# Kernel optimization log

Hardware: AMD Instinct MI355X
Metric: run time of the kernel (lower is better)

Reference implementation:

```python
import jax, jax.numpy as jnp
import numpy as np

V, E, H2, K = 30000, 256, 256, 13  # vocab, embed dim, per-direction hidden, num tags
B, T = 64, 512


def setup_inputs() -> dict:
    key = jax.random.key(0)
    ks = jax.random.split(key, 12)
    s = 0.1
    return {
        "x": jax.random.randint(ks[0], (B, T), 0, V, dtype=jnp.int32),
        "emb": jax.random.normal(ks[1], (V, E), dtype=jnp.float32) * s,
        "w_ih_f": jax.random.normal(ks[2], (4 * H2, E), dtype=jnp.float32) * s,
        "w_hh_f": jax.random.normal(ks[3], (4 * H2, H2), dtype=jnp.float32) * s,
        "b_ih_f": jnp.zeros((4 * H2,), jnp.float32),
        "b_hh_f": jnp.zeros((4 * H2,), jnp.float32),
        "w_ih_b": jax.random.normal(ks[4], (4 * H2, E), dtype=jnp.float32) * s,
        "w_hh_b": jax.random.normal(ks[5], (4 * H2, H2), dtype=jnp.float32) * s,
        "b_ih_b": jnp.zeros((4 * H2,), jnp.float32),
        "b_hh_b": jnp.zeros((4 * H2,), jnp.float32),
        "w_out": jax.random.normal(ks[6], (K, 2 * H2), dtype=jnp.float32) * s,
        "b_out": jnp.zeros((K,), jnp.float32),
        "start_trans": jax.random.normal(ks[7], (K,), dtype=jnp.float32) * s,
        "end_trans": jax.random.normal(ks[8], (K,), dtype=jnp.float32) * s,
        "trans": jax.random.normal(ks[9], (K, K), dtype=jnp.float32) * s,
    }


def _lstm_dir(xg, w_hh, reverse):
    # xg: [T, B, 4H] precomputed input-side gate pre-activations (PyTorch i|f|g|o order)
    Bsz, H = xg.shape[1], w_hh.shape[1]

    def step(carry, g_in):
        h, c = carry
        g = g_in + h @ w_hh.T
        i, f, gg, o = jnp.split(g, 4, axis=-1)
        c = jax.nn.sigmoid(f) * c + jax.nn.sigmoid(i) * jnp.tanh(gg)
        h = jax.nn.sigmoid(o) * jnp.tanh(c)
        return (h, c), h

    init = (jnp.zeros((Bsz, H), xg.dtype), jnp.zeros((Bsz, H), xg.dtype))
    _, hs = jax.lax.scan(step, init, xg, reverse=reverse)
    return hs  # [T, B, H]


def reference(x, emb, w_ih_f, w_hh_f, b_ih_f, b_hh_f, w_ih_b, w_hh_b, b_ih_b, b_hh_b,
              w_out, b_out, start_trans, end_trans, trans):
    e = emb[x].transpose(1, 0, 2)                     # [T, B, E] time-major
    xg_f = e @ w_ih_f.T + (b_ih_f + b_hh_f)           # [T, B, 4H] (fold both biases)
    xg_b = e @ w_ih_b.T + (b_ih_b + b_hh_b)
    h_f = _lstm_dir(xg_f, w_hh_f, reverse=False)
    h_b = _lstm_dir(xg_b, w_hh_b, reverse=True)
    h = jnp.concatenate([h_f, h_b], axis=-1)          # [T, B, 2H]; dropout = identity (eval)
    emissions = h @ w_out.T + b_out                   # [T, B, K]

    # CRF Viterbi decode (torchcrf semantics, full mask)
    score = start_trans + emissions[0]                # [B, K]

    def vstep(score, emit_t):
        s = score[:, :, None] + trans[None] + emit_t[:, None, :]  # [B, K_prev, K_next]
        return s.max(axis=1), s.argmax(axis=1)

    score, bps = jax.lax.scan(vstep, score, emissions[1:])        # bps: [T-1, B, K]
    score = score + end_trans
    best_last = jnp.argmax(score, axis=-1)            # [B]
    best_score = jnp.max(score, axis=-1)              # [B]

    def btstep(tag, bp_t):
        prev = jnp.take_along_axis(bp_t, tag[:, None], axis=1)[:, 0]
        return prev, prev

    _, path_head = jax.lax.scan(btstep, best_last, bps, reverse=True)  # [T-1, B]
    path = jnp.concatenate([path_head, best_last[None]], axis=0).T     # [B, T]
    return path, best_score
```

## Files before the change

kernel.cpp:

```cpp
#include <hip/hip_runtime.h>
#include <stdint.h>
#include <stddef.h>

#define T_LEN  512
#define BATCH  64
#define NTAG   13
#define CT     64
#define NCHUNK 8
#define CTS    128
#define NSC    4

__device__ __forceinline__ float sigm(float x) { return 1.0f / (1.0f + expf(-x)); }

__global__ __launch_bounds__(256) void xg_gemm4(
    const int* __restrict__ x, const float* __restrict__ emb,
    const float* __restrict__ w_ih_f, const float* __restrict__ w_ih_b,
    const float* __restrict__ b_ih_f, const float* __restrict__ b_hh_f,
    const float* __restrict__ b_ih_b, const float* __restrict__ b_hh_b,
    float* __restrict__ xg_ws, int sch)
{
    const int tid = threadIdx.x;
    const int mt = blockIdx.x;
    const int nt = blockIdx.y;
    const int d  = blockIdx.z;
    const int tbase = (d == 0 ? sch : (NSC - 1 - sch)) * CTS;
    const float* W  = (d == 0) ? w_ih_f : w_ih_b;
    const float* bi = (d == 0) ? b_ih_f : b_ih_b;
    const float* bh = (d == 0) ? b_hh_f : b_hh_b;

    __shared__ __align__(16) float Wl[16][260];
    __shared__ __align__(16) float El[16][132];
    __shared__ int tok[128];

    if (tid < 128) {
        int col = nt * 128 + tid;
        tok[tid] = x[(col & 63) * T_LEN + tbase + (col >> 6)];
    }
    __syncthreads();

    const int r  = tid;
    const int er = tid >> 1;
    const int c8 = (tid & 1) * 8;
    const int tg = tid >> 4;
    const int tn = tid & 15;

    float acc[16][8];
#pragma unroll
    for (int i = 0; i < 16; i++)
#pragma unroll
        for (int jz = 0; jz < 8; jz++) acc[i][jz] = 0.0f;

    const float* wrow = &W[(size_t)(mt * 256 + r) * 256];
    const float* erow = &emb[(size_t)tok[er] * 256];

    for (int kb = 0; kb < 256; kb += 16) {
        float4 w0 = *(const float4*)&wrow[kb + 0];
        float4 w1 = *(const float4*)&wrow[kb + 4];
        float4 w2 = *(const float4*)&wrow[kb + 8];
        float4 w3 = *(const float4*)&wrow[kb + 12];
        float4 e0 = *(const float4*)&erow[kb + c8];
        float4 e1 = *(const float4*)&erow[kb + c8 + 4];
        __syncthreads();
        Wl[ 0][r] = w0.x; Wl[ 1][r] = w0.y; Wl[ 2][r] = w0.z; Wl[ 3][r] = w0.w;
        Wl[ 4][r] = w1.x; Wl[ 5][r] = w1.y; Wl[ 6][r] = w1.z; Wl[ 7][r] = w1.w;
        Wl[ 8][r] = w2.x; Wl[ 9][r] = w2.y; Wl[10][r] = w2.z; Wl[11][r] = w2.w;
        Wl[12][r] = w3.x; Wl[13][r] = w3.y; Wl[14][r] = w3.z; Wl[15][r] = w3.w;
        El[c8+0][er] = e0.x; El[c8+1][er] = e0.y; El[c8+2][er] = e0.z; El[c8+3][er] = e0.w;
        El[c8+4][er] = e1.x; El[c8+5][er] = e1.y; El[c8+6][er] = e1.z; El[c8+7][er] = e1.w;
        __syncthreads();
#pragma unroll
        for (int kk = 0; kk < 16; kk++) {
            float a[16], b[8];
            *(float4*)&a[ 0] = *(const float4*)&Wl[kk][tg*16 +  0];
            *(float4*)&a[ 4] = *(const float4*)&Wl[kk][tg*16 +  4];
            *(float4*)&a[ 8] = *(const float4*)&Wl[kk][tg*16 +  8];
            *(float4*)&a[12] = *(const float4*)&Wl[kk][tg*16 + 12];
            *(float4*)&b[0]  = *(const float4*)&El[kk][tn*8];
            *(float4*)&b[4]  = *(const float4*)&El[kk][tn*8 + 4];
#pragma unroll
            for (int i = 0; i < 16; i++)
#pragma unroll
                for (int jz = 0; jz < 8; jz++)
                    acc[i][jz] += a[i] * b[jz];
        }
    }

    const int colbase = nt * 128 + tn * 8;
    const int j  = colbase >> 6;
    const int b0 = colbase & 63;
#pragma unroll
    for (int gi = 0; gi < 16; gi++) {
        int g = mt * 256 + tg * 16 + gi;
        float bias = bi[g] + bh[g];
        float* dst = &xg_ws[(((size_t)(d * CTS + j) * 1024 + g) << 6) + b0];
        float4 v0 = make_float4(acc[gi][0]+bias, acc[gi][1]+bias, acc[gi][2]+bias, acc[gi][3]+bias);
        float4 v1 = make_float4(acc[gi][4]+bias, acc[gi][5]+bias, acc[gi][6]+bias, acc[gi][7]+bias);
        *(float4*)dst       = v0;
        *(float4*)(dst + 4) = v1;
    }
}

__global__ __launch_bounds__(256) void lstm_chunk4(
    const float* __restrict__ xg_ws,
    const float* __restrict__ w_hh_f, const float* __restrict__ w_hh_b,
    float* h_ex, float* c_state, float* h_all, int* flags, int sch)
{
    const int tid = threadIdx.x;
    const int bid = blockIdx.x;
    const int dg    = bid & 7;
    const int slice = bid >> 3;
    const int dir = dg & 1;
    const int grp = dg >> 1;
    const int h_base = slice * 8;
    const int sbase  = grp * 16;

    __shared__ __align__(16) float w_lds[32][260];
    __shared__ __align__(16) float h_lds[16][260];
    __shared__ __align__(16) float red[7][32][20];
    __shared__ float gatebuf[32][17];

    const float* W = dir ? w_hh_b : w_hh_f;
    for (int idx = tid; idx < 2048; idx += 256) {
        int f  = idx << 2;
        int rr = f >> 8;
        int c4 = f & 255;
        int row = (rr >> 3) * 256 + h_base + (rr & 7);
        *(float4*)&w_lds[rr][c4] = *(const float4*)&W[(size_t)row * 256 + c4];
    }

    const int ih_g = tid & 7;
    const int s_g  = tid >> 3;
    float c_val = 0.0f;
    if (tid < 128)
        c_val = c_state[(size_t)(dir * 64 + sbase + s_g) * 256 + h_base + ih_g];

    {
        const float* base = &h_ex[((size_t)dg * 16) * 256];
#pragma unroll
        for (int i = 0; i < 8; i++) {
            int pos = tid + 256 * i;
            int fo  = pos << 1;
            unsigned long long u64 = __hip_atomic_load(
                (const unsigned long long*)(base + fo), __ATOMIC_RELAXED, __HIP_MEMORY_SCOPE_AGENT);
            float2 v = __builtin_bit_cast(float2, u64);
            *(float2*)&h_lds[fo >> 8][fo & 255] = v;
        }
    }
    __syncthreads();

    const int kc   = tid >> 5;
    const int tile = tid & 31;
    const int gt = tile >> 2;
    const int st = tile & 3;
    const float* wr[4] = { &w_lds[gt][0], &w_lds[8+gt][0], &w_lds[16+gt][0], &w_lds[24+gt][0] };
    const float* hr[4] = { &h_lds[st][0], &h_lds[4+st][0], &h_lds[8+st][0],  &h_lds[12+st][0] };

    float hv_prev = 0.0f;
    size_t ha_prev = 0;

#pragma unroll 1
    for (int tl = 0; tl < CTS; tl++) {
        const int jslot = dir ? (CTS - 1 - tl) : tl;
        const int t = (dir ? (NSC - 1 - sch) : sch) * CTS + jslot;
        const int sc = sch * CTS + tl + 1;
        const int par = sc & 1;

        float xg0 = 0.f, xg1 = 0.f, xg2 = 0.f, xg3 = 0.f;
        if (tid < 128) {
            if (tl > 0) h_all[ha_prev] = hv_prev;
            const float* xp = &xg_ws[(((size_t)(dir * CTS + jslot) * 1024) + h_base + ih_g) * 64 + sbase + s_g];
            xg0 = xp[0];
            xg1 = xp[1 * 256 * 64];
            xg2 = xp[2 * 256 * 64];
            xg3 = xp[3 * 256 * 64];
        }

        float acc[4][4];
#pragma unroll
        for (int gi = 0; gi < 4; gi++)
#pragma unroll
            for (int si = 0; si < 4; si++) acc[gi][si] = 0.0f;

        const int j0 = kc * 32;
#pragma unroll
        for (int m = 0; m < 8; m++) {
            const int jj = j0 + m * 4;
            float4 w4[4], h4[4];
#pragma unroll
            for (int i = 0; i < 4; i++) w4[i] = *(const float4*)(wr[i] + jj);
#pragma unroll
            for (int i = 0; i < 4; i++) h4[i] = *(const float4*)(hr[i] + jj);
#pragma unroll
            for (int gi = 0; gi < 4; gi++)
#pragma unroll
                for (int si = 0; si < 4; si++)
                    acc[gi][si] += w4[gi].x*h4[si].x + w4[gi].y*h4[si].y
                                 + w4[gi].z*h4[si].z + w4[gi].w*h4[si].w;
        }

        if (kc >= 1) {
#pragma unroll
            for (int gi = 0; gi < 4; gi++)
                *(float4*)&red[kc-1][tile][gi*4] =
                    make_float4(acc[gi][0], acc[gi][1], acc[gi][2], acc[gi][3]);
        }
        __syncthreads();
        if (kc == 0) {
#pragma unroll
            for (int p = 0; p < 7; p++)
#pragma unroll
                for (int gi = 0; gi < 4; gi++) {
                    float4 v = *(const float4*)&red[p][tile][gi*4];
                    acc[gi][0] += v.x; acc[gi][1] += v.y; acc[gi][2] += v.z; acc[gi][3] += v.w;
                }
#pragma unroll
            for (int gi = 0; gi < 4; gi++)
#pragma unroll
                for (int si = 0; si < 4; si++)
                    gatebuf[8*gi + gt][4*si + st] = acc[gi][si];
        }
        __syncthreads();

        if (tid < 128) {
            float gI = gatebuf[     ih_g][s_g] + xg0;
            float gF = gatebuf[8  + ih_g][s_g] + xg1;
            float gG = gatebuf[16 + ih_g][s_g] + xg2;
            float gO = gatebuf[24 + ih_g][s_g] + xg3;
            c_val = sigm(gF) * c_val + sigm(gI) * tanhf(gG);
            float hv = sigm(gO) * tanhf(c_val);
            __hip_atomic_store(&h_ex[(((size_t)par * 8 + dg) * 16 + s_g) * 256 + h_base + ih_g],
                               hv, __ATOMIC_RELAXED, __HIP_MEMORY_SCOPE_AGENT);
            hv_prev = hv;
            ha_prev = ((size_t)t * 64 + sbase + s_g) * 512 + dir * 256 + h_base + ih_g;
        }
        __syncthreads();

        if (tid == 0)
            __hip_atomic_store(&flags[dg * 32 + slice], sc, __ATOMIC_RELAXED, __HIP_MEMORY_SCOPE_AGENT);

        if (tid < 64) {
            const int* fp = &flags[dg * 32 + (tid & 31)];
            int spins = 0;
            int v = __hip_atomic_load(fp, __ATOMIC_RELAXED, __HIP_MEMORY_SCOPE_AGENT);
            while (__ballot(v < sc) != 0ull) {
                if (++spins > 8) __builtin_amdgcn_s_sleep(1);
                v = __hip_atomic_load(fp, __ATOMIC_RELAXED, __HIP_MEMORY_SCOPE_AGENT);
                if (spins > (1 << 20)) break;
            }
        }
        __syncthreads();

        {
            const float* base = &h_ex[(((size_t)par * 8 + dg) * 16) * 256];
#pragma unroll
            for (int i = 0; i < 8; i++) {
                int pos = tid + 256 * i;
                int fo  = pos << 1;
                unsigned long long u64 = __hip_atomic_load(
                    (const unsigned long long*)(base + fo), __ATOMIC_RELAXED, __HIP_MEMORY_SCOPE_AGENT);
                float2 v = __builtin_bit_cast(float2, u64);
                *(float2*)&h_lds[fo >> 8][fo & 255] = v;
            }
        }
        __syncthreads();
    }

    if (tid < 128) {
        h_all[ha_prev] = hv_prev;
        c_state[(size_t)(dir * 64 + sbase + s_g) * 256 + h_base + ih_g] = c_val;
    }
}

__global__ __launch_bounds__(256) void emis_kernel(
    const float* __restrict__ h_all, const float* __restrict__ w_out,
    const float* __restrict__ b_out, float* __restrict__ emis)
{
    const int row = blockIdx.x * 16 + (threadIdx.x >> 4);
    const int k   = threadIdx.x & 15;
    const float* hr = &h_all[(size_t)row * 512];
    const float* wr = &w_out[(size_t)(k < NTAG ? k : 0) * 512];
    float acc = 0.0f;
#pragma unroll 8
    for (int e = 0; e < 512; e += 4) {
        float4 h4 = *(const float4*)&hr[e];
        float4 w4 = *(const float4*)&wr[e];
        acc += h4.x*w4.x + h4.y*w4.y + h4.z*w4.z + h4.w*w4.w;
    }
    if (k < NTAG) emis[(size_t)row * NTAG + k] = acc + b_out[k];
}

__global__ __launch_bounds__(64) void viterbi_kernel(
    const float* __restrict__ emis, const float* __restrict__ start_trans,
    const float* __restrict__ end_trans, const float* __restrict__ trans,
    float* __restrict__ out)
{
    const int b = blockIdx.x;
    const int k = threadIdx.x;
    __shared__ float em[T_LEN * NTAG];
    __shared__ unsigned char bp[T_LEN][16];

    for (int t = k; t < T_LEN; t += 64) {
        const float* src = &emis[((size_t)t * 64 + b) * NTAG];
#pragma unroll
        for (int kk = 0; kk < NTAG; kk++)
            em[t * NTAG + kk] = src[kk];
    }
    __syncthreads();

    float tc[NTAG];
#pragma unroll
    for (int kp = 0; kp < NTAG; kp++)
        tc[kp] = (k < NTAG) ? trans[kp * NTAG + k] : 0.0f;

    float score = (k < NTAG) ? (start_trans[k] + em[k]) : -3.0e38f;

    for (int t = 1; t < T_LEN; t++) {
        float best = -3.0e38f;
        int bi = 0;
#pragma unroll
        for (int kp = 0; kp < NTAG; kp++) {
            float v = __shfl(score, kp) + tc[kp];
            if (v > best) { best = v; bi = kp; }
        }
        if (k < NTAG) {
            score = best + em[t * NTAG + k];
            bp[t][k] = (unsigned char)bi;
        }
    }
    if (k < NTAG) score += end_trans[k];
    else score = -3.0e38f;
    __syncthreads();

    float bs = -3.0e38f;
    int tag = 0;
#pragma unroll
    for (int kk = 0; kk < NTAG; kk++) {
        float v = __shfl(score, kk);
        if (v > bs) { bs = v; tag = kk; }
    }
    if (k == 0) {
        out[32768 + b] = bs;
        int tg = tag;
        out[b * T_LEN + (T_LEN - 1)] = (float)tg;
        for (int t = T_LEN - 1; t >= 1; t--) {
            tg = bp[t][tg];
            out[b * T_LEN + t - 1] = (float)tg;
        }
    }
}

extern "C" void kernel_launch(void* const* d_in, const int* in_sizes, int n_in,
                              void* d_out, int out_size, void* d_ws, size_t ws_size,
                              hipStream_t stream)
{
    (void)in_sizes; (void)n_in; (void)out_size; (void)ws_size;
    const int*   x    = (const int*)  d_in[0];
    const float* emb  = (const float*)d_in[1];
    const float* wihf = (const float*)d_in[2];
    const float* whhf = (const float*)d_in[3];
    const float* bihf = (const float*)d_in[4];
    const float* bhhf = (const float*)d_in[5];
    const float* wihb = (const float*)d_in[6];
    const float* whhb = (const float*)d_in[7];
    const float* bihb = (const float*)d_in[8];
    const float* bhhb = (const float*)d_in[9];
    const float* wout = (const float*)d_in[10];
    const float* bout = (const float*)d_in[11];
    const float* stt  = (const float*)d_in[12];
    const float* ent  = (const float*)d_in[13];
    const float* trn  = (const float*)d_in[14];
    float* out = (float*)d_out;

    const size_t XG4_BYTES   = (size_t)2 * CTS * 1024 * 64 * 4;
    const size_t HALL_BYTES  = (size_t)T_LEN * 64 * 512 * 4;
    const size_t HEX_BYTES   = (size_t)2 * 8 * 16 * 256 * 4;
    const size_t CST_BYTES   = (size_t)2 * 64 * 256 * 4;
    const size_t EMIS_BYTES  = (size_t)T_LEN * 64 * NTAG * 4;
    const size_t FLAG_BYTES  = 8 * 32 * 4;

    char* ws = (char*)d_ws;
    size_t off = 0;
    float* xg_ws = (float*)(ws + off); off += XG4_BYTES;
    float* h_all = (float*)(ws + off); off += HALL_BYTES;
    float* h_ex  = (float*)(ws + off); off += HEX_BYTES;
    float* c_st  = (float*)(ws + off); off += CST_BYTES;
    float* emis  = (float*)(ws + off); off += EMIS_BYTES;
    int*   flags = (int*)  (ws + off); off += FLAG_BYTES;

    hipMemsetAsync(h_ex,  0, HEX_BYTES, stream);
    hipMemsetAsync(c_st,  0, CST_BYTES, stream);
    hipMemsetAsync(flags, 0, FLAG_BYTES, stream);

    for (int c = 0; c < NSC; c++) {
        xg_gemm4<<<dim3(4, 64, 2), 256, 0, stream>>>(x, emb, wihf, wihb,
                                                     bihf, bhhf, bihb, bhhb, xg_ws, c);
        lstm_chunk4<<<256, 256, 0, stream>>>(xg_ws, whhf, whhb, h_ex, c_st, h_all, flags, c);
    }
    emis_kernel<<<2048, 256, 0, stream>>>(h_all, wout, bout, emis);
    viterbi_kernel<<<64, 64, 0, stream>>>(emis, stt, ent, trn, out);
}
```

Baseline: 3.381 ms.

## Enlarge xg GEMM tile to 256x256 with register prefetch and merge memsets

The input-projection GEMM now computes a 256-column tile per block, with a 16x16 micro-tile per thread instead of 16x8, which halves the grid in y. The next k-slice of weights and embeddings is prefetched into registers while the current slice is computed from LDS, overlapping global loads with math. Three small memsets are merged into one by making the workspace buffers contiguous. The cost is more accumulator registers, which may lower occupancy, and fewer blocks per launch.

New measurement: 3.605 ms. +6.6%, slower.

```diff
diff --git a/kernel.cpp b/kernel.cpp
--- a/kernel.cpp
+++ b/kernel.cpp
@@ -29,74 +29,94 @@
     const float* bh = (d == 0) ? b_hh_f : b_hh_b;
 
     __shared__ __align__(16) float Wl[16][260];
-    __shared__ __align__(16) float El[16][132];
-    __shared__ int tok[128];
-
-    if (tid < 128) {
-        int col = nt * 128 + tid;
-        tok[tid] = x[(col & 63) * T_LEN + tbase + (col >> 6)];
+    __shared__ __align__(16) float El[16][16][20];
+    __shared__ int tok[256];
+
+    {
+        int c = nt * 256 + tid;
+        tok[tid] = x[(c & 63) * T_LEN + tbase + (c >> 6)];
     }
     __syncthreads();
 
-    const int r  = tid;
-    const int er = tid >> 1;
-    const int c8 = (tid & 1) * 8;
     const int tg = tid >> 4;
     const int tn = tid & 15;
 
-    float acc[16][8];
+    float acc[16][16];
 #pragma unroll
     for (int i = 0; i < 16; i++)
 #pragma unroll
-        for (int jz = 0; jz < 8; jz++) acc[i][jz] = 0.0f;
-
-    const float* wrow = &W[(size_t)(mt * 256 + r) * 256];
-    const float* erow = &emb[(size_t)tok[er] * 256];
+        for (int jz = 0; jz < 16; jz++) acc[i][jz] = 0.0f;
+
+    const float* wrow = &W[(size_t)(mt * 256 + tid) * 256];
+    const float* erow = &emb[(size_t)tok[tid] * 256];
+
+    float4 w0 = *(const float4*)&wrow[0];
+    float4 w1 = *(const float4*)&wrow[4];
+    float4 w2 = *(const float4*)&wrow[8];
+    float4 w3 = *(const float4*)&wrow[12];
+    float4 e0 = *(const float4*)&erow[0];
+    float4 e1 = *(const float4*)&erow[4];
+    float4 e2 = *(const float4*)&erow[8];
+    float4 e3 = *(const float4*)&erow[12];
+
+    const int ecg = tid >> 4;
+    const int ecw = tid & 15;
 
     for (int kb = 0; kb < 256; kb += 16) {
-        float4 w0 = *(const float4*)&wrow[kb + 0];
-        float4 w1 = *(const float4*)&wrow[kb + 4];
-        float4 w2 = *(const float4*)&wrow[kb + 8];
-        float4 w3 = *(const float4*)&wrow[kb + 12];
-        float4 e0 = *(const float4*)&erow[kb + c8];
-        float4 e1 = *(const float4*)&erow[kb + c8 + 4];
-        __syncthreads();
-        Wl[ 0][r] = w0.x; Wl[ 1][r] = w0.y; Wl[ 2][r] = w0.z; Wl[ 3][r] = w0.w;
-        Wl[ 4][r] = w1.x; Wl[ 5][r] = w1.y; Wl[ 6][r] = w1.z; Wl[ 7][r] = w1.w;
-        Wl[ 8][r] = w2.x; Wl[ 9][r] = w2.y; Wl[10][r] = w2.z; Wl[11][r] = w2.w;
-        Wl[12][r] = w3.x; Wl[13][r] = w3.y; Wl[14][r] = w3.z; Wl[15][r] = w3.w;
-        El[c8+0][er] = e0.x; El[c8+1][er] = e0.y; El[c8+2][er] = e0.z; El[c8+3][er] = e0.w;
-        El[c8+4][er] = e1.x; El[c8+5][er] = e1.y; El[c8+6][er] = e1.z; El[c8+7][er] = e1.w;
-        __syncthreads();
+        __syncthreads();
+        Wl[ 0][tid] = w0.x; Wl[ 1][tid] = w0.y; Wl[ 2][tid] = w0.z; Wl[ 3][tid] = w0.w;
+        Wl[ 4][tid] = w1.x; Wl[ 5][tid] = w1.y; Wl[ 6][tid] = w1.z; Wl[ 7][tid] = w1.w;
+        Wl[ 8][tid] = w2.x; Wl[ 9][tid] = w2.y; Wl[10][tid] = w2.z; Wl[11][tid] = w2.w;
+        Wl[12][tid] = w3.x; Wl[13][tid] = w3.y; Wl[14][tid] = w3.z; Wl[15][tid] = w3.w;
+        El[ 0][ecg][ecw] = e0.x; El[ 1][ecg][ecw] = e0.y; El[ 2][ecg][ecw] = e0.z; El[ 3][ecg][ecw] = e0.w;
+        El[ 4][ecg][ecw] = e1.x; El[ 5][ecg][ecw] = e1.y; El[ 6][ecg][ecw] = e1.z; El[ 7][ecg][ecw] = e1.w;
+        El[ 8][ecg][ecw] = e2.x; El[ 9][ecg][ecw] = e2.y; El[10][ecg][ecw] = e2.z; El[11][ecg][ecw] = e2.w;
+        El[12][ecg][ecw] = e3.x; El[13][ecg][ecw] = e3.y; El[14][ecg][ecw] = e3.z; El[15][ecg][ecw] = e3.w;
+        __syncthreads();
+
+        if (kb + 16 < 256) {
+            w0 = *(const float4*)&wrow[kb + 16 + 0];
+            w1 = *(const float4*)&wrow[kb + 16 + 4];
+            w2 = *(const float4*)&wrow[kb + 16 + 8];
+            w3 = *(const float4*)&wrow[kb + 16 + 12];
+            e0 = *(const float4*)&erow[kb + 16 + 0];
+            e1 = *(const float4*)&erow[kb + 16 + 4];
+            e2 = *(const float4*)&erow[kb + 16 + 8];
+            e3 = *(const float4*)&erow[kb + 16 + 12];
+        }
+
 #pragma unroll
         for (int kk = 0; kk < 16; kk++) {
-            float a[16], b[8];
+            float a[16], b[16];
             *(float4*)&a[ 0] = *(const float4*)&Wl[kk][tg*16 +  0];
             *(float4*)&a[ 4] = *(const float4*)&Wl[kk][tg*16 +  4];
             *(float4*)&a[ 8] = *(const float4*)&Wl[kk][tg*16 +  8];
             *(float4*)&a[12] = *(const float4*)&Wl[kk][tg*16 + 12];
-            *(float4*)&b[0]  = *(const float4*)&El[kk][tn*8];
-            *(float4*)&b[4]  = *(const float4*)&El[kk][tn*8 + 4];
+            *(float4*)&b[ 0] = *(const float4*)&El[kk][tn][ 0];
+            *(float4*)&b[ 4] = *(const float4*)&El[kk][tn][ 4];
+            *(float4*)&b[ 8] = *(const float4*)&El[kk][tn][ 8];
+            *(float4*)&b[12] = *(const float4*)&El[kk][tn][12];
 #pragma unroll
             for (int i = 0; i < 16; i++)
 #pragma unroll
-                for (int jz = 0; jz < 8; jz++)
+                for (int jz = 0; jz < 16; jz++)
                     acc[i][jz] += a[i] * b[jz];
         }
     }
 
-    const int colbase = nt * 128 + tn * 8;
-    const int j  = colbase >> 6;
-    const int b0 = colbase & 63;
+    const int j  = nt * 4 + (tn >> 2);
+    const int b0 = (tn & 3) * 16;
 #pragma unroll
     for (int gi = 0; gi < 16; gi++) {
         int g = mt * 256 + tg * 16 + gi;
         float bias = bi[g] + bh[g];
         float* dst = &xg_ws[(((size_t)(d * CTS + j) * 1024 + g) << 6) + b0];
-        float4 v0 = make_float4(acc[gi][0]+bias, acc[gi][1]+bias, acc[gi][2]+bias, acc[gi][3]+bias);
-        float4 v1 = make_float4(acc[gi][4]+bias, acc[gi][5]+bias, acc[gi][6]+bias, acc[gi][7]+bias);
-        *(float4*)dst       = v0;
-        *(float4*)(dst + 4) = v1;
+#pragma unroll
+        for (int q = 0; q < 4; q++) {
+            float4 v = make_float4(acc[gi][q*4+0]+bias, acc[gi][q*4+1]+bias,
+                                   acc[gi][q*4+2]+bias, acc[gi][q*4+3]+bias);
+            *(float4*)(dst + q*4) = v;
+        }
     }
 }
 
@@ -375,8 +395,8 @@
     const size_t HALL_BYTES  = (size_t)T_LEN * 64 * 512 * 4;
     const size_t HEX_BYTES   = (size_t)2 * 8 * 16 * 256 * 4;
     const size_t CST_BYTES   = (size_t)2 * 64 * 256 * 4;
+    const size_t FLAG_BYTES  = 8 * 32 * 4;
     const size_t EMIS_BYTES  = (size_t)T_LEN * 64 * NTAG * 4;
-    const size_t FLAG_BYTES  = 8 * 32 * 4;
 
     char* ws = (char*)d_ws;
     size_t off = 0;
@@ -384,15 +404,13 @@
     float* h_all = (float*)(ws + off); off += HALL_BYTES;
     float* h_ex  = (float*)(ws + off); off += HEX_BYTES;
     float* c_st  = (float*)(ws + off); off += CST_BYTES;
+    int*   flags = (int*)  (ws + off); off += FLAG_BYTES;
     float* emis  = (float*)(ws + off); off += EMIS_BYTES;
-    int*   flags = (int*)  (ws + off); off += FLAG_BYTES;
-
-    hipMemsetAsync(h_ex,  0, HEX_BYTES, stream);
-    hipMemsetAsync(c_st,  0, CST_BYTES, stream);
-    hipMemsetAsync(flags, 0, FLAG_BYTES, stream);
+
+    hipMemsetAsync(h_ex, 0, HEX_BYTES + CST_BYTES + FLAG_BYTES, stream);
 
     for (int c = 0; c < NSC; c++) {
-        xg_gemm4<<<dim3(4, 64, 2), 256, 0, stream>>>(x, emb, wihf, wihb,
+        xg_gemm4<<<dim3(4, 32, 2), 256, 0, stream>>>(x, emb, wihf, wihb,
                                                      bihf, bhhf, bihb, bhhb, xg_ws, c);
         lstm_chunk4<<<256, 256, 0, stream>>>(xg_ws, whhf, whhb, h_ex, c_st, h_all, flags, c);
     }
```
